# Kernel tuning notes

Measured on AMD Instinct MI355X. Metric: run time of the kernel, lower is better.

The kernel has to match this reference:

```python
import jax, jax.numpy as jnp
import numpy as np

N_WIRES = 5
N_OPS = 100000
BATCH = 64
TWO_PI = 6.283185307179586


def _apply_1q(state, U, axis):
    # Apply a shared 2x2 unitary U to the given wire axis of state [B,2,2,2,2,2].
    s = jnp.moveaxis(state, axis, -1)
    s = jnp.einsum('ij,...j->...i', U, s)
    return jnp.moveaxis(s, -1, axis)


def _apply_1q_batched(state, U, axis):
    # Per-batch 2x2 unitaries U: [B,2,2].
    s = jnp.moveaxis(state, axis, -1)
    s = jnp.einsum('bij,b...j->b...i', U, s)
    return jnp.moveaxis(s, -1, axis)


def _rot_unitaries(angles, types):
    # Build [n_ops,2,2] complex64 unitaries: type 0 -> RX, 1 -> RY, 2 -> RZ.
    half = angles * 0.5
    c = jnp.cos(half).astype(jnp.complex64)
    s = jnp.sin(half).astype(jnp.complex64)
    mis = (-1j) * s
    Urx = jnp.stack([jnp.stack([c, mis], -1), jnp.stack([mis, c], -1)], -2)
    Ury = jnp.stack([jnp.stack([c, -s], -1), jnp.stack([s, c], -1)], -2)
    e = jnp.exp((-1j) * half)  # complex64
    zero = jnp.zeros_like(e)
    Urz = jnp.stack([jnp.stack([e, zero], -1), jnp.stack([zero, jnp.conj(e)], -1)], -2)
    t = types[:, None, None]
    return jnp.where(t == 0, Urx, jnp.where(t == 1, Ury, Urz))


def _forward(x, gate_angles, gate_wires, gate_types):
    B = x.shape[0]
    # |00000> initial state per batch item
    state = jnp.zeros((B,) + (2,) * N_WIRES, jnp.complex64)
    state = state.at[(slice(None),) + (0,) * N_WIRES].set(1.0)

    # RxEncoder: RX(x[:, k]) on wire k
    half = x * 0.5
    c = jnp.cos(half).astype(jnp.complex64)
    s = jnp.sin(half).astype(jnp.complex64)
    for k in range(N_WIRES):
        U = jnp.stack([jnp.stack([c[:, k], (-1j) * s[:, k]], -1),
                       jnp.stack([(-1j) * s[:, k], c[:, k]], -1)], -2)  # [B,2,2]
        state = _apply_1q_batched(state, U, k + 1)

    # RandomLayer: long sequential chain of tiny gates on a resident state vector
    Us = _rot_unitaries(gate_angles, gate_types)
    branches = [lambda st, U, a=k + 1: _apply_1q(st, U, a) for k in range(N_WIRES)]

    def step(st, inp):
        U, w = inp
        return jax.lax.switch(w, branches, st, U), None

    state, _ = jax.lax.scan(step, state, (Us, gate_wires))

    # Measure: expval of PauliY on every wire -> [B, 5]
    Y = jnp.array([[0.0, -1j], [1j, 0.0]], jnp.complex64)
    outs = []
    for k in range(N_WIRES):
        ys = _apply_1q(state, Y, k + 1)
        outs.append(jnp.sum(jnp.conj(state) * ys, axis=tuple(range(1, N_WIRES + 1))).real)
    return jnp.stack(outs, -1)


def setup_inputs() -> dict:
    key = jax.random.key(0)
    k1, k2, k3, k4 = jax.random.split(key, 4)
    x = jax.random.normal(k1, (BATCH, N_WIRES), dtype=jnp.float32)
    gate_angles = jax.random.uniform(k2, (N_OPS,), dtype=jnp.float32) * TWO_PI
    gate_wires = jax.random.randint(k3, (N_OPS,), 0, N_WIRES, dtype=jnp.int32)
    gate_types = jax.random.randint(k4, (N_OPS,), 0, 3, dtype=jnp.int32)
    return {"x": x, "gate_angles": gate_angles, "gate_wires": gate_wires, "gate_types": gate_types}


def reference(x, gate_angles, gate_wires, gate_types):
    return _forward(x, gate_angles, gate_wires, gate_types)
```

## Files before the change

kernel.cpp:

```cpp
#include <hip/hip_runtime.h>

#define N_WIRES 5
#define BATCH 64

#define BLOCKS_A 64
#define THREADS_A 256
#define LANES (BLOCKS_A * THREADS_A)
#define TUP (N_WIRES * 8)

__device__ __forceinline__ void cmatmul(float* r, const float* B, const float* A) {
    r[0] = B[0]*A[0] - B[1]*A[1] + B[2]*A[4] - B[3]*A[5];
    r[1] = B[0]*A[1] + B[1]*A[0] + B[2]*A[5] + B[3]*A[4];
    r[2] = B[0]*A[2] - B[1]*A[3] + B[2]*A[6] - B[3]*A[7];
    r[3] = B[0]*A[3] + B[1]*A[2] + B[2]*A[7] + B[3]*A[6];
    r[4] = B[4]*A[0] - B[5]*A[1] + B[6]*A[4] - B[7]*A[5];
    r[5] = B[4]*A[1] + B[5]*A[0] + B[6]*A[5] + B[7]*A[4];
    r[6] = B[4]*A[2] - B[5]*A[3] + B[6]*A[6] - B[7]*A[7];
    r[7] = B[4]*A[3] + B[5]*A[2] + B[6]*A[7] + B[7]*A[6];
}

__global__ __launch_bounds__(THREADS_A)
void gate_partials(const float* __restrict__ angles,
                   const int*   __restrict__ wires,
                   const int*   __restrict__ types,
                   int n_ops, int chunk,
                   float* __restrict__ ws)
{
    const int lane = blockIdx.x * THREADS_A + threadIdx.x;

    float acc[N_WIRES][8];
    #pragma unroll
    for (int w = 0; w < N_WIRES; ++w) {
        acc[w][0] = 1.f; acc[w][1] = 0.f; acc[w][2] = 0.f; acc[w][3] = 0.f;
        acc[w][4] = 0.f; acc[w][5] = 0.f; acc[w][6] = 1.f; acc[w][7] = 0.f;
    }

    const int g0 = lane * chunk;
    const int g1 = min(g0 + chunk, n_ops);
    for (int g = g0; g < g1; ++g) {
        const float ang = angles[g];
        const int   w   = wires[g];
        const int   t   = types[g];
        float s, c;
        __sincosf(0.5f * ang, &s, &c);
        const float na = (t == 2) ? -s : 0.f;
        const float nb = (t == 1) ? -s : 0.f;
        const float ng = (t == 0) ? -s : 0.f;
        #pragma unroll
        for (int k = 0; k < N_WIRES; ++k) {
            if (w == k) {
                float* m = acc[k];
                const float m00r =  c*m[0] - na*m[1] + nb*m[4] - ng*m[5];
                const float m00i =  c*m[1] + na*m[0] + nb*m[5] + ng*m[4];
                const float m01r =  c*m[2] - na*m[3] + nb*m[6] - ng*m[7];
                const float m01i =  c*m[3] + na*m[2] + nb*m[7] + ng*m[6];
                const float m10r = -nb*m[0] - ng*m[1] + c*m[4] + na*m[5];
                const float m10i = -nb*m[1] + ng*m[0] + c*m[5] - na*m[4];
                const float m11r = -nb*m[2] - ng*m[3] + c*m[6] + na*m[7];
                const float m11i = -nb*m[3] + ng*m[2] + c*m[7] - na*m[6];
                m[0]=m00r; m[1]=m00i; m[2]=m01r; m[3]=m01i;
                m[4]=m10r; m[5]=m10i; m[6]=m11r; m[7]=m11i;
            }
        }
    }

    __shared__ float lds[THREADS_A][TUP];
    #pragma unroll
    for (int i = 0; i < TUP; ++i) lds[threadIdx.x][i] = acc[i >> 3][i & 7];
    __syncthreads();
    for (int st = 1; st < THREADS_A; st <<= 1) {
        if ((threadIdx.x & (2*st - 1)) == 0) {
            #pragma unroll
            for (int w = 0; w < N_WIRES; ++w) {
                float r[8];
                cmatmul(r, &lds[threadIdx.x + st][w*8], &lds[threadIdx.x][w*8]);
                #pragma unroll
                for (int i = 0; i < 8; ++i) lds[threadIdx.x][w*8 + i] = r[i];
            }
        }
        __syncthreads();
    }
    if (threadIdx.x == 0) {
        #pragma unroll
        for (int i = 0; i < TUP; ++i) ws[blockIdx.x * TUP + i] = lds[0][i];
    }
}

__global__ __launch_bounds__(320)
void finalize(const float* __restrict__ x,
              const float* __restrict__ ws,
              float* __restrict__ out)
{
    __shared__ float red[BLOCKS_A][TUP];
    const int tid = threadIdx.x;
    if (tid < BLOCKS_A) {
        #pragma unroll
        for (int i = 0; i < TUP; ++i) red[tid][i] = ws[tid * TUP + i];
    }
    __syncthreads();
    for (int st = 1; st < BLOCKS_A; st <<= 1) {
        if (tid < BLOCKS_A && (tid & (2*st - 1)) == 0) {
            #pragma unroll
            for (int w = 0; w < N_WIRES; ++w) {
                float r[8];
                cmatmul(r, &red[tid + st][w*8], &red[tid][w*8]);
                #pragma unroll
                for (int i = 0; i < 8; ++i) red[tid][w*8 + i] = r[i];
            }
        }
        __syncthreads();
    }

    if (tid < BATCH * N_WIRES) {
        const int b = tid / N_WIRES;
        const int k = tid % N_WIRES;
        const float xv = x[b * N_WIRES + k];
        float sx, cx;
        __sincosf(0.5f * xv, &sx, &cx);
        const float* U = &red[0][k*8];
        const float v0r = cx*U[0] + sx*U[3];
        const float v0i = cx*U[1] - sx*U[2];
        const float v1r = cx*U[4] + sx*U[7];
        const float v1i = cx*U[5] - sx*U[6];
        out[tid] = 2.f * (v0r * v1i - v0i * v1r);
    }
}

extern "C" void kernel_launch(void* const* d_in, const int* in_sizes, int n_in,
                              void* d_out, int out_size, void* d_ws, size_t ws_size,
                              hipStream_t stream) {
    const float* x      = (const float*)d_in[0];
    const float* angles = (const float*)d_in[1];
    const int*   wires  = (const int*)d_in[2];
    const int*   types  = (const int*)d_in[3];
    float* out = (float*)d_out;
    float* ws  = (float*)d_ws;

    const int n_ops = in_sizes[1];
    const int chunk = (n_ops + LANES - 1) / LANES;

    gate_partials<<<BLOCKS_A, THREADS_A, 0, stream>>>(angles, wires, types, n_ops, chunk, ws);
    finalize<<<1, 320, 0, stream>>>(x, ws, out);
}
```

Before: 80.74 us.

## Represent per-wire SU(2) accumulators as quaternions and reduce with wave shuffles

```diff
diff --git a/kernel.cpp b/kernel.cpp
--- a/kernel.cpp
+++ b/kernel.cpp
@@ -1,22 +1,32 @@
 #include <hip/hip_runtime.h>
+
 
 #define N_WIRES 5
 #define BATCH 64
-
 #define BLOCKS_A 64
 #define THREADS_A 256
 #define LANES (BLOCKS_A * THREADS_A)
-#define TUP (N_WIRES * 8)
+#define QTUP (N_WIRES * 4)
 
-__device__ __forceinline__ void cmatmul(float* r, const float* B, const float* A) {
-    r[0] = B[0]*A[0] - B[1]*A[1] + B[2]*A[4] - B[3]*A[5];
-    r[1] = B[0]*A[1] + B[1]*A[0] + B[2]*A[5] + B[3]*A[4];
-    r[2] = B[0]*A[2] - B[1]*A[3] + B[2]*A[6] - B[3]*A[7];
-    r[3] = B[0]*A[3] + B[1]*A[2] + B[2]*A[7] + B[3]*A[6];
-    r[4] = B[4]*A[0] - B[5]*A[1] + B[6]*A[4] - B[7]*A[5];
-    r[5] = B[4]*A[1] + B[5]*A[0] + B[6]*A[5] + B[7]*A[4];
-    r[6] = B[4]*A[2] - B[5]*A[3] + B[6]*A[6] - B[7]*A[7];
-    r[7] = B[4]*A[3] + B[5]*A[2] + B[6]*A[7] + B[7]*A[6];
+__device__ __forceinline__ void qmul(float* r, const float* b, const float* a) {
+    r[0] = b[0]*a[0] - b[1]*a[1] - b[2]*a[2] - b[3]*a[3];
+    r[1] = b[0]*a[1] + b[1]*a[0] + b[2]*a[3] - b[3]*a[2];
+    r[2] = b[0]*a[2] - b[1]*a[3] + b[2]*a[0] + b[3]*a[1];
+    r[3] = b[0]*a[3] + b[1]*a[2] - b[2]*a[1] + b[3]*a[0];
+}
+
+__device__ __forceinline__ void wave_reduce6(float* t) {
+    for (int st = 1; st < 64; st <<= 1) {
+        float o[QTUP];
+        #pragma unroll
+        for (int i = 0; i < QTUP; ++i) o[i] = __shfl_down(t[i], st, 64);
+        #pragma unroll
+        for (int w = 0; w < N_WIRES; ++w) {
+            float r[4];
+            qmul(r, &o[4*w], &t[4*w]);
+            t[4*w+0] = r[0]; t[4*w+1] = r[1]; t[4*w+2] = r[2]; t[4*w+3] = r[3];
+        }
+    }
 }
 
 __global__ __launch_bounds__(THREADS_A)
@@ -28,11 +38,10 @@
 {
     const int lane = blockIdx.x * THREADS_A + threadIdx.x;
 
-    float acc[N_WIRES][8];
+    float acc[N_WIRES][4];
     #pragma unroll
     for (int w = 0; w < N_WIRES; ++w) {
         acc[w][0] = 1.f; acc[w][1] = 0.f; acc[w][2] = 0.f; acc[w][3] = 0.f;
-        acc[w][4] = 0.f; acc[w][5] = 0.f; acc[w][6] = 1.f; acc[w][7] = 0.f;
     }
 
     const int g0 = lane * chunk;
@@ -43,46 +52,57 @@
         const int   t   = types[g];
         float s, c;
         __sincosf(0.5f * ang, &s, &c);
-        const float na = (t == 2) ? -s : 0.f;
-        const float nb = (t == 1) ? -s : 0.f;
-        const float ng = (t == 0) ? -s : 0.f;
+
+        float qw = acc[0][0], qx = acc[0][1], qy = acc[0][2], qz = acc[0][3];
+        #pragma unroll
+        for (int k = 1; k < N_WIRES; ++k) {
+            const bool m = (w == k);
+            qw = m ? acc[k][0] : qw;  qx = m ? acc[k][1] : qx;
+            qy = m ? acc[k][2] : qy;  qz = m ? acc[k][3] : qz;
+        }
+        const float pw = (t == 0) ? -qx : (t == 1) ? -qy : -qz;
+        const float px = (t == 0) ?  qw : (t == 1) ?  qz : -qy;
+        const float py = (t == 0) ? -qz : (t == 1) ?  qw :  qx;
+        const float pz = (t == 0) ?  qy : (t == 1) ? -qx :  qw;
+        const float nw = c*qw + s*pw;
+        const float nx = c*qx + s*px;
+        const float ny = c*qy + s*py;
+        const float nz = c*qz + s*pz;
         #pragma unroll
         for (int k = 0; k < N_WIRES; ++k) {
-            if (w == k) {
-                float* m = acc[k];
-                const float m00r =  c*m[0] - na*m[1] + nb*m[4] - ng*m[5];
-                const float m00i =  c*m[1] + na*m[0] + nb*m[5] + ng*m[4];
-                const float m01r =  c*m[2] - na*m[3] + nb*m[6] - ng*m[7];
-                const float m01i =  c*m[3] + na*m[2] + nb*m[7] + ng*m[6];
-                const float m10r = -nb*m[0] - ng*m[1] + c*m[4] + na*m[5];
-                const float m10i = -nb*m[1] + ng*m[0] + c*m[5] - na*m[4];
-                const float m11r = -nb*m[2] - ng*m[3] + c*m[6] + na*m[7];
-                const float m11i = -nb*m[3] + ng*m[2] + c*m[7] - na*m[6];
-                m[0]=m00r; m[1]=m00i; m[2]=m01r; m[3]=m01i;
-                m[4]=m10r; m[5]=m10i; m[6]=m11r; m[7]=m11i;
-            }
+            const bool m = (w == k);
+            acc[k][0] = m ? nw : acc[k][0];  acc[k][1] = m ? nx : acc[k][1];
+            acc[k][2] = m ? ny : acc[k][2];  acc[k][3] = m ? nz : acc[k][3];
         }
     }
 
-    __shared__ float lds[THREADS_A][TUP];
+    float t[QTUP];
     #pragma unroll
-    for (int i = 0; i < TUP; ++i) lds[threadIdx.x][i] = acc[i >> 3][i & 7];
+    for (int i = 0; i < QTUP; ++i) t[i] = acc[i >> 2][i & 3];
+    wave_reduce6(t);
+
+    __shared__ float lds[4][QTUP];
+    const int wave = threadIdx.x >> 6;
+    if ((threadIdx.x & 63) == 0) {
+        #pragma unroll
+        for (int i = 0; i < QTUP; ++i) lds[wave][i] = t[i];
+    }
     __syncthreads();
-    for (int st = 1; st < THREADS_A; st <<= 1) {
-        if ((threadIdx.x & (2*st - 1)) == 0) {
+    if (threadIdx.x == 0) {
+        float r[QTUP];
+        #pragma unroll
+        for (int i = 0; i < QTUP; ++i) r[i] = lds[0][i];
+        #pragma unroll
+        for (int v = 1; v < 4; ++v) {
             #pragma unroll
             for (int w = 0; w < N_WIRES; ++w) {
-                float r[8];
-                cmatmul(r, &lds[threadIdx.x + st][w*8], &lds[threadIdx.x][w*8]);
-                #pragma unroll
-                for (int i = 0; i < 8; ++i) lds[threadIdx.x][w*8 + i] = r[i];
+                float z[4];
+                qmul(z, &lds[v][4*w], &r[4*w]);
+                r[4*w+0] = z[0]; r[4*w+1] = z[1]; r[4*w+2] = z[2]; r[4*w+3] = z[3];
             }
         }
-        __syncthreads();
-    }
-    if (threadIdx.x == 0) {
         #pragma unroll
-        for (int i = 0; i < TUP; ++i) ws[blockIdx.x * TUP + i] = lds[0][i];
+        for (int i = 0; i < QTUP; ++i) ws[blockIdx.x * QTUP + i] = r[i];
     }
 }
 
@@ -91,25 +111,19 @@
               const float* __restrict__ ws,
               float* __restrict__ out)
 {
-    __shared__ float red[BLOCKS_A][TUP];
+    __shared__ float U[QTUP];
     const int tid = threadIdx.x;
-    if (tid < BLOCKS_A) {
+    if (tid < 64) {
+        float t[QTUP];
         #pragma unroll
-        for (int i = 0; i < TUP; ++i) red[tid][i] = ws[tid * TUP + i];
+        for (int i = 0; i < QTUP; ++i) t[i] = ws[tid * QTUP + i];
+        wave_reduce6(t);
+        if (tid == 0) {
+            #pragma unroll
+            for (int i = 0; i < QTUP; ++i) U[i] = t[i];
+        }
     }
     __syncthreads();
-    for (int st = 1; st < BLOCKS_A; st <<= 1) {
-        if (tid < BLOCKS_A && (tid & (2*st - 1)) == 0) {
-            #pragma unroll
-            for (int w = 0; w < N_WIRES; ++w) {
-                float r[8];
-                cmatmul(r, &red[tid + st][w*8], &red[tid][w*8]);
-                #pragma unroll
-                for (int i = 0; i < 8; ++i) red[tid][w*8 + i] = r[i];
-            }
-        }
-        __syncthreads();
-    }
 
     if (tid < BATCH * N_WIRES) {
         const int b = tid / N_WIRES;
@@ -117,11 +131,11 @@
         const float xv = x[b * N_WIRES + k];
         float sx, cx;
         __sincosf(0.5f * xv, &sx, &cx);
-        const float* U = &red[0][k*8];
-        const float v0r = cx*U[0] + sx*U[3];
-        const float v0i = cx*U[1] - sx*U[2];
-        const float v1r = cx*U[4] + sx*U[7];
-        const float v1i = cx*U[5] - sx*U[6];
+        const float* q = &U[4*k];
+        const float v0r =  cx*q[0] - sx*q[1];
+        const float v0i = -cx*q[3] + sx*q[2];
+        const float v1r =  cx*q[2] + sx*q[3];
+        const float v1i = -cx*q[1] - sx*q[0];
         out[tid] = 2.f * (v0r * v1i - v0i * v1r);
     }
 }
```

Result: faster. 67.37 us (-16.6%).
